# Optimization experiments

Hardware: AMD Instinct MI355X
Metric: run time of the kernel (lower is better)

The kernel has to match this reference:

```python
import jax, jax.numpy as jnp
import numpy as np
import math

B, H, S, D = 4, 16, 2048, 128

def setup_inputs() -> dict:
    key = jax.random.key(0)
    kq, kk, kv = jax.random.split(key, 3)
    query = jax.random.normal(kq, (B, H, S, D), dtype=jnp.float32)
    k = jax.random.normal(kk, (B, H, S, D), dtype=jnp.float32)
    value = jax.random.normal(kv, (B, H, S, D), dtype=jnp.float32)
    attn_mask = jnp.tril(jnp.ones((S, S), dtype=bool))  # causal
    key_padding_mask = jnp.ones((B, S), dtype=bool)      # all keys valid
    return {"query": query, "key": k, "value": value,
            "attn_mask": attn_mask, "key_padding_mask": key_padding_mask}

def reference(query, key, value, attn_mask, key_padding_mask):
    dk = query.shape[-1]
    # [B,H,Sq,Sk]
    scores = jnp.einsum('bhqd,bhkd->bhqk', query, key) / math.sqrt(dk)
    fill = jnp.finfo(scores.dtype).min
    # attn_mask [Sq,Sk] -> [1,1,Sq,Sk]; True = keep
    scores = jnp.where(attn_mask[None, None, :, :], scores, fill)
    # key_padding_mask [B,Sk] -> [B,1,1,Sk]; True = keep
    scores = jnp.where(key_padding_mask[:, None, None, :], scores, fill)
    attn = jax.nn.softmax(scores, axis=-1)
    # dropout p=0.0 / eval mode -> identity
    return jnp.einsum('bhqk,bhkd->bhqd', attn, value)
```

## Files before the change

### kernel.cpp

```cpp
#include <hip/hip_runtime.h>
#include <hip/hip_bf16.h>
#include <math.h>

#define S_LEN 2048
#define D_DIM 128
#define NHEADS 64

typedef unsigned short u16;
typedef __attribute__((ext_vector_type(8))) short bf16x8;
typedef __attribute__((ext_vector_type(4))) float f32x4;
typedef __attribute__((ext_vector_type(16))) float f32x16;

__device__ __forceinline__ u16 f2b(float f) {
  union { float f; unsigned u; } v; v.f = f;
  return (u16)((v.u + 0x7fffu + ((v.u >> 16) & 1u)) >> 16);
}
__device__ __forceinline__ unsigned cvtpk(float lo, float hi) {
  unsigned r;
  asm("v_cvt_pk_bf16_f32 %0, %1, %2" : "=v"(r) : "v"(lo), "v"(hi));
  return r;
}
__device__ __forceinline__ void pl32swap(unsigned &a, unsigned &b) {
  asm("v_permlane32_swap_b32 %0, %1" : "+v"(a), "+v"(b));
}
__device__ __forceinline__ f32x16 z16() {
  f32x16 v;
  #pragma unroll
  for (int i = 0; i < 16; ++i) v[i] = 0.f;
  return v;
}

#define GLL16(g, l) __builtin_amdgcn_global_load_lds(                       \
    (const __attribute__((address_space(1))) unsigned*)(g),                 \
    (__attribute__((address_space(3))) unsigned*)(l), 16, 0, 0)

__global__ __launch_bounds__(256, 2)
void conv_kernel(const float* __restrict__ K, const float* __restrict__ V,
                 u16* __restrict__ Kws, u16* __restrict__ Vws) {
  __shared__ float VLf[128 * 65];
  const int h = blockIdx.x >> 3;
  const int s = blockIdx.x & 7;
  const int tid = threadIdx.x;
  const size_t hb = (size_t)h * S_LEN * D_DIM;
  const float* Kb = K + hb;
  const float* Vb = V + hb;
  u16* Ko = Kws + hb;
  u16* Vo = Vws + hb;

  #pragma unroll 2
  for (int it = 0; it < 16; ++it) {
    int idx = it * 256 + tid;
    int k = 256 * s + (idx >> 4), g = idx & 15;
    const float* src = Kb + (size_t)k * D_DIM + 8 * g;
    float4 a = *(const float4*)src;
    float4 b = *(const float4*)(src + 4);
    bf16x8 f;
    f[0]=f2b(a.x); f[1]=f2b(a.y); f[2]=f2b(a.z); f[3]=f2b(a.w);
    f[4]=f2b(b.x); f[5]=f2b(b.y); f[6]=f2b(b.z); f[7]=f2b(b.w);
    *(bf16x8*)&Ko[(size_t)k * D_DIM + 8 * g] = f;
  }
  for (int tt = 0; tt < 4; ++tt) {
    const int k0t = 256 * s + 64 * tt;
    __syncthreads();
    #pragma unroll 2
    for (int it = 0; it < 8; ++it) {
      int idx = it * 256 + tid;
      int row = idx >> 5, c4 = idx & 31;
      float4 v = *(const float4*)(Vb + (size_t)(k0t + row) * D_DIM + 4 * c4);
      VLf[(4*c4 + 0) * 65 + row] = v.x;
      VLf[(4*c4 + 1) * 65 + row] = v.y;
      VLf[(4*c4 + 2) * 65 + row] = v.z;
      VLf[(4*c4 + 3) * 65 + row] = v.w;
    }
    __syncthreads();
    #pragma unroll
    for (int it = 0; it < 4; ++it) {
      int idx = it * 256 + tid;
      int d = idx >> 3, kc = idx & 7;
      const float* src = &VLf[d * 65 + 8 * kc];
      bf16x8 f;
      #pragma unroll
      for (int j = 0; j < 8; ++j) f[j] = f2b(src[j]);
      *(bf16x8*)&Vo[(size_t)d * S_LEN + k0t + 8 * kc] = f;
    }
  }
}

__global__ __launch_bounds__(512, 2)
void fattn8w(const float* __restrict__ Qg, const u16* __restrict__ Kws,
             const u16* __restrict__ Vws, float* __restrict__ Og) {
  __shared__ __align__(16) u16 Kl[2][8192];
  __shared__ __align__(16) u16 Vl[2][8192];

  const int tid = threadIdx.x, lane = tid & 63, w = tid >> 6;
  const int l31 = lane & 31, hi = lane >> 5;
  const int kx = l31 & 7;

  const int b = blockIdx.x;
  const int xcd = b & 7, slot = b >> 3;
  const int head = xcd * 8 + (slot & 7);
  const int qsel = slot >> 3;
  const int qmap[8] = {7, 5, 6, 4, 0, 2, 1, 3};
  const int qt = qmap[qsel];

  const size_t hb = (size_t)head * S_LEN * D_DIM;
  const float* Qb = Qg + hb;
  float*       Ob = Og + hb;
  const u16*   Kh = Kws + hb;
  const u16*   Vh = Vws + hb;

  auto stage = [&](int buf, int t) {
    const int k0 = t * 64;
    #pragma unroll
    for (int j = 0; j < 2; ++j) {
      const int sb = (w * 2 + j) * 64;
      {
        int sk = sb + lane;
        int k = sk >> 4, gs = sk & 15, g = gs ^ (k & 7);
        GLL16(Kh + (size_t)(k0 + k) * D_DIM + 8 * g, &Kl[buf][sb * 8]);
      }
      {
        int sv = sb + lane;
        int d = sv >> 3, gks = sv & 7, gk = gks ^ (d & 7);
        GLL16(Vh + (size_t)d * S_LEN + k0 + 8 * gk, &Vl[buf][sb * 8]);
      }
    }
  };

#define CHUNK(SV, CB, CI)                                                   \
  do {                                                                      \
    float p0 = exp2f((SV)[(CB)+0] - m_run), p1 = exp2f((SV)[(CB)+1] - m_run); \
    float p2 = exp2f((SV)[(CB)+2] - m_run), p3 = exp2f((SV)[(CB)+3] - m_run); \
    float p4 = exp2f((SV)[(CB)+4] - m_run), p5 = exp2f((SV)[(CB)+5] - m_run); \
    float p6 = exp2f((SV)[(CB)+6] - m_run), p7 = exp2f((SV)[(CB)+7] - m_run); \
    psA += (p0 + p1) + (p2 + p3);                                           \
    psB += (p4 + p5) + (p6 + p7);                                           \
    unsigned a0 = cvtpk(p0, p1), a1 = cvtpk(p2, p3);                        \
    unsigned a2 = cvtpk(p4, p5), a3 = cvtpk(p6, p7);                        \
    pl32swap(a0, a2); pl32swap(a1, a3);                                     \
    union { unsigned u[4]; bf16x8 v; } pf_;                                 \
    pf_.u[0] = a0; pf_.u[1] = a1; pf_.u[2] = a2; pf_.u[3] = a3;             \
    const int gv = ((CI) * 2 + hi) ^ kx;                                    \
    bf16x8 v0 = *(const bf16x8*)&V8[( l31      ) * 64 + gv * 8];            \
    bf16x8 v1 = *(const bf16x8*)&V8[( 32 + l31 ) * 64 + gv * 8];            \
    bf16x8 v2 = *(const bf16x8*)&V8[( 64 + l31 ) * 64 + gv * 8];            \
    bf16x8 v3 = *(const bf16x8*)&V8[( 96 + l31 ) * 64 + gv * 8];            \
    __builtin_amdgcn_s_setprio(1);                                          \
    oa0 = __builtin_amdgcn_mfma_f32_32x32x16_bf16(v0, pf_.v, oa0, 0,0,0);   \
    oa1 = __builtin_amdgcn_mfma_f32_32x32x16_bf16(v1, pf_.v, oa1, 0,0,0);   \
    oa2 = __builtin_amdgcn_mfma_f32_32x32x16_bf16(v2, pf_.v, oa2, 0,0,0);   \
    oa3 = __builtin_amdgcn_mfma_f32_32x32x16_bf16(v3, pf_.v, oa3, 0,0,0);   \
    __builtin_amdgcn_s_setprio(0);                                          \
  } while (0)

  const int q0w = qt * 256 + 32 * w;
  const int ntk = 4 * qt + 4;
  const int myq = q0w + l31;

  stage(0, 0);

  bf16x8 qf[8];
  {
    const float sc = 0.12753139f;
    const float* qp = Qb + (size_t)myq * D_DIM + 8 * hi;
    #pragma unroll
    for (int c = 0; c < 8; ++c) {
      float4 a = *(const float4*)(qp + 16 * c);
      float4 b2 = *(const float4*)(qp + 16 * c + 4);
      bf16x8 f;
      f[0]=f2b(a.x*sc);  f[1]=f2b(a.y*sc);  f[2]=f2b(a.z*sc);  f[3]=f2b(a.w*sc);
      f[4]=f2b(b2.x*sc); f[5]=f2b(b2.y*sc); f[6]=f2b(b2.z*sc); f[7]=f2b(b2.w*sc);
      qf[c] = f;
    }
  }

  f32x16 oa0 = z16(), oa1 = z16(), oa2 = z16(), oa3 = z16();
  float m_run = 0.f, l_run = 0.f;

  #pragma unroll 1
  for (int t = 0; t < ntk; ++t) {
    asm volatile("s_waitcnt vmcnt(0)" ::: "memory");
    __builtin_amdgcn_s_barrier();
    asm volatile("" ::: "memory");
    if (t + 1 < ntk) stage((t + 1) & 1, t + 1);

    if (64 * t <= q0w + 31) {
      const u16* K8 = &Kl[t & 1][0];
      const u16* V8 = &Vl[t & 1][0];

      f32x16 s0 = z16(), s1 = z16();
      __builtin_amdgcn_s_setprio(1);
      #pragma unroll
      for (int c = 0; c < 8; ++c) {
        const int gs = (c * 2 + hi) ^ kx;
        bf16x8 ka = *(const bf16x8*)&K8[ l31       * 128 + gs * 8];
        bf16x8 kb = *(const bf16x8*)&K8[(32 + l31) * 128 + gs * 8];
        s0 = __builtin_amdgcn_mfma_f32_32x32x16_bf16(ka, qf[c], s0, 0,0,0);
        s1 = __builtin_amdgcn_mfma_f32_32x32x16_bf16(kb, qf[c], s1, 0,0,0);
      }
      __builtin_amdgcn_s_setprio(0);

      if (64 * t + 63 > q0w) {
        const int qm = myq - 64 * t;
        #pragma unroll
        for (int i = 0; i < 16; ++i) {
          const int kr = (i & 3) + 8 * (i >> 2) + 4 * hi;
          if (kr > qm)      s0[i] = -1e30f;
          if (32 + kr > qm) s1[i] = -1e30f;
        }
      }

      float tm[16];
      #pragma unroll
      for (int i = 0; i < 16; ++i) tm[i] = fmaxf(s0[i], s1[i]);
      #pragma unroll
      for (int st = 8; st >= 1; st >>= 1)
        #pragma unroll
        for (int i = 0; i < 8; ++i) if (i < st) tm[i] = fmaxf(tm[i], tm[i+st]);
      float mx = fmaxf(tm[0], __shfl_xor(tm[0], 32));

      if (mx > m_run + 8.0f) {
        float corr = exp2f(m_run - mx);
        #pragma unroll
        for (int i = 0; i < 16; ++i) {
          oa0[i] *= corr; oa1[i] *= corr; oa2[i] *= corr; oa3[i] *= corr;
        }
        l_run *= corr; m_run = mx;
      }

      float psA = 0.f, psB = 0.f;
      CHUNK(s0, 0, 0);
      CHUNK(s0, 8, 1);
      CHUNK(s1, 0, 2);
      CHUNK(s1, 8, 3);
      l_run += psA + psB;
    }
  }

  float l_tot = l_run + __shfl_xor(l_run, 32);
  float inv = 1.0f / l_tot;
  float* op = Ob + (size_t)myq * D_DIM;
  #pragma unroll
  for (int bq = 0; bq < 4; ++bq) {
    const int d0 = 8 * bq + 4 * hi;
    *(float4*)(op + d0) =
      make_float4(oa0[4*bq]*inv, oa0[4*bq+1]*inv, oa0[4*bq+2]*inv, oa0[4*bq+3]*inv);
    *(float4*)(op + 32 + d0) =
      make_float4(oa1[4*bq]*inv, oa1[4*bq+1]*inv, oa1[4*bq+2]*inv, oa1[4*bq+3]*inv);
    *(float4*)(op + 64 + d0) =
      make_float4(oa2[4*bq]*inv, oa2[4*bq+1]*inv, oa2[4*bq+2]*inv, oa2[4*bq+3]*inv);
    *(float4*)(op + 96 + d0) =
      make_float4(oa3[4*bq]*inv, oa3[4*bq+1]*inv, oa3[4*bq+2]*inv, oa3[4*bq+3]*inv);
  }
#undef CHUNK
}

__global__ __launch_bounds__(256, 3)
void fattn_v2(const float* __restrict__ Qg, const float* __restrict__ Kg,
              const float* __restrict__ Vg, float* __restrict__ Og) {
  __shared__ __align__(16) u16 K8[16 * 64 * 8];
  __shared__ __align__(16) u16 V8[8 * 128 * 8];
  __shared__ __align__(16) u16 Plf[4 * 16 * 72];
  const int tid = threadIdx.x, lane = tid & 63, w = tid >> 6;
  const int lr = lane & 15, lg = lane >> 4;
  const int qtile = blockIdx.x % 32, bh = blockIdx.x / 32;
  const int q0 = qtile * 64;
  const size_t base = (size_t)bh * S_LEN * D_DIM;
  const float *Qb = Qg + base, *Kb = Kg + base, *Vb = Vg + base;
  float* Ob = Og + base;
  bf16x8 qf[4];
  {
    const float* qp = Qb + (size_t)(q0 + w * 16 + lr) * D_DIM + lg * 8;
    #pragma unroll
    for (int cc = 0; cc < 4; ++cc) {
      float4 a = *(const float4*)(qp + cc * 32);
      float4 b = *(const float4*)(qp + cc * 32 + 4);
      bf16x8 f;
      f[0]=f2b(a.x); f[1]=f2b(a.y); f[2]=f2b(a.z); f[3]=f2b(a.w);
      f[4]=f2b(b.x); f[5]=f2b(b.y); f[6]=f2b(b.z); f[7]=f2b(b.w);
      qf[cc] = f;
    }
  }
  f32x4 oacc[8];
  #pragma unroll
  for (int c = 0; c < 8; ++c) oacc[c] = (f32x4){0.f,0.f,0.f,0.f};
  float m_run[4] = {-INFINITY,-INFINITY,-INFINITY,-INFINITY};
  float l_run[4] = {0.f,0.f,0.f,0.f};
  const int sg_ = tid >> 5, dq_ = tid & 31;
  float4 kb[8], vb[8];
  auto prefetch = [&](int k0) {
    const float* kp = Kb + (size_t)(k0 + lane) * D_DIM;
    #pragma unroll
    for (int i = 0; i < 4; ++i) {
      int dg = w + 4 * i;
      kb[2*i]   = *(const float4*)(kp + dg * 8);
      kb[2*i+1] = *(const float4*)(kp + dg * 8 + 4);
    }
    #pragma unroll
    for (int jj = 0; jj < 8; ++jj) {
      int row = k0 + (jj & 3) * 16 + 2 * sg_ + (jj >> 2);
      vb[jj] = *(const float4*)(Vb + (size_t)row * D_DIM + dq_ * 4);
    }
  };
  const int ntiles = qtile + 1;
  const float scale = 0.08838834764831845f;
  prefetch(0);
  for (int t = 0; t < ntiles; ++t) {
    #pragma unroll
    for (int i = 0; i < 4; ++i) {
      int dg = w + 4 * i;
      float4 a = kb[2*i], b = kb[2*i+1];
      bf16x8 f;
      f[0]=f2b(a.x); f[1]=f2b(a.y); f[2]=f2b(a.z); f[3]=f2b(a.w);
      f[4]=f2b(b.x); f[5]=f2b(b.y); f[6]=f2b(b.z); f[7]=f2b(b.w);
      *(bf16x8*)&K8[(dg * 64 + lane) * 8] = f;
    }
    #pragma unroll
    for (int dd = 0; dd < 4; ++dd) {
      bf16x8 f;
      #pragma unroll
      for (int jj = 0; jj < 8; ++jj) {
        float c = (dd==0)?vb[jj].x:(dd==1)?vb[jj].y:(dd==2)?vb[jj].z:vb[jj].w;
        f[jj] = f2b(c);
      }
      *(bf16x8*)&V8[(sg_ * 128 + dq_ * 4 + dd) * 8] = f;
    }
    __syncthreads();
    if (t + 1 < ntiles) prefetch((t + 1) * 64);
    const bool diag = (t == qtile);
    f32x4 sa[4];
    #pragma unroll
    for (int c = 0; c < 4; ++c) sa[c] = (f32x4){0.f,0.f,0.f,0.f};
    #pragma unroll
    for (int cc = 0; cc < 4; ++cc) {
      #pragma unroll
      for (int c = 0; c < 4; ++c) {
        bf16x8 kf = *(const bf16x8*)&K8[((cc*4+lg)*64 + c*16 + lr)*8];
        sa[c] = __builtin_amdgcn_mfma_f32_16x16x32_bf16(qf[cc], kf, sa[c], 0,0,0);
      }
    }
    #pragma unroll
    for (int r = 0; r < 4; ++r) {
      float s0=sa[0][r]*scale, s1=sa[1][r]*scale, s2=sa[2][r]*scale, s3=sa[3][r]*scale;
      if (diag) {
        int lim = 16*w + lg*4 + r;
        if (     lr > lim) s0 = -INFINITY;
        if (16 + lr > lim) s1 = -INFINITY;
        if (32 + lr > lim) s2 = -INFINITY;
        if (48 + lr > lim) s3 = -INFINITY;
      }
      float mx = fmaxf(fmaxf(s0,s1), fmaxf(s2,s3));
      #pragma unroll
      for (int d = 1; d < 16; d <<= 1) mx = fmaxf(mx, __shfl_xor(mx, d));
      float mn = fmaxf(m_run[r], mx);
      float corr = __expf(m_run[r] - mn);
      float p0=__expf(s0-mn), p1=__expf(s1-mn), p2=__expf(s2-mn), p3=__expf(s3-mn);
      float ps = (p0+p1)+(p2+p3);
      #pragma unroll
      for (int d = 1; d < 16; d <<= 1) ps += __shfl_xor(ps, d);
      l_run[r] = l_run[r]*corr + ps;
      m_run[r] = mn;
      #pragma unroll
      for (int c = 0; c < 8; ++c) oacc[c][r] *= corr;
      ushort4 pw = make_ushort4(f2b(p0), f2b(p1), f2b(p2), f2b(p3));
      *(ushort4*)&Plf[((w*16 + lg*4 + r) * 72) + 4*lr] = pw;
    }
    #pragma unroll
    for (int pass = 0; pass < 2; ++pass) {
      bf16x8 pfv = *(const bf16x8*)&Plf[(w*16 + lr)*72 + pass*32 + lg*8];
      #pragma unroll
      for (int c = 0; c < 8; ++c) {
        bf16x8 vf = *(const bf16x8*)&V8[((pass*4 + lg)*128 + c*16 + lr)*8];
        oacc[c] = __builtin_amdgcn_mfma_f32_16x16x32_bf16(pfv, vf, oacc[c], 0,0,0);
      }
    }
    __syncthreads();
  }
  #pragma unroll
  for (int r = 0; r < 4; ++r) {
    const int mq = q0 + w*16 + lg*4 + r;
    const float inv = 1.0f / l_run[r];
    float* op = Ob + (size_t)mq * D_DIM + lr;
    #pragma unroll
    for (int c = 0; c < 8; ++c) op[c*16] = oacc[c][r] * inv;
  }
}

extern "C" void kernel_launch(void* const* d_in, const int* in_sizes, int n_in,
                              void* d_out, int out_size, void* d_ws, size_t ws_size,
                              hipStream_t stream) {
  const float* Q = (const float*)d_in[0];
  const float* K = (const float*)d_in[1];
  const float* V = (const float*)d_in[2];
  float* O = (float*)d_out;
  const size_t elems = (size_t)NHEADS * S_LEN * D_DIM;
  const size_t need = 2 * elems * sizeof(u16);
  if (ws_size >= need) {
    u16* Kws = (u16*)d_ws;
    u16* Vws = Kws + elems;
    conv_kernel<<<dim3(512), dim3(256), 0, stream>>>(K, V, Kws, Vws);
    fattn8w<<<dim3(512), dim3(512), 0, stream>>>(Q, Kws, Vws, O);
  } else {
    fattn_v2<<<dim3(NHEADS * 32), dim3(256), 0, stream>>>(Q, K, V, O);
  }
}
```

Baseline: 172.4 us.

## Switch flash attention to 4-wave blocks with 32-key tiles

Replaces the 8-wave, 256-query-per-block kernel with a 4-wave kernel covering 128 queries per block, launched as 1024 blocks. Each step now processes 32 keys instead of 64, which halves LDS buffers and lets more blocks share a CU. It also replaces the XCD-aware head mapping with a simpler head index plus a causal-balancing query-tile order. The trade-off is more loop iterations and barriers per key and less K/V reuse per staged tile, and the XCD-local L2 grouping of heads is lost.

New measurement: 365.0 us. 112% more time.

```diff
diff --git a/kernel.cpp b/kernel.cpp
--- a/kernel.cpp
+++ b/kernel.cpp
@@ -86,22 +86,22 @@
   }
 }
 
-__global__ __launch_bounds__(512, 2)
-void fattn8w(const float* __restrict__ Qg, const u16* __restrict__ Kws,
+__global__ __launch_bounds__(256, 4)
+void fattn4w(const float* __restrict__ Qg, const u16* __restrict__ Kws,
              const u16* __restrict__ Vws, float* __restrict__ Og) {
-  __shared__ __align__(16) u16 Kl[2][8192];
-  __shared__ __align__(16) u16 Vl[2][8192];
+  __shared__ __align__(16) u16 Kl[2][4096];
+  __shared__ __align__(16) u16 Vl[2][4096];
 
   const int tid = threadIdx.x, lane = tid & 63, w = tid >> 6;
   const int l31 = lane & 31, hi = lane >> 5;
   const int kx = l31 & 7;
+  const int vx = (l31 >> 1) & 3;
 
   const int b = blockIdx.x;
-  const int xcd = b & 7, slot = b >> 3;
-  const int head = xcd * 8 + (slot & 7);
-  const int qsel = slot >> 3;
-  const int qmap[8] = {7, 5, 6, 4, 0, 2, 1, 3};
-  const int qt = qmap[qsel];
+  const int head = b & 63;
+  const int qsel = b >> 6;
+  const int g = qsel >> 2, i = qsel & 3;
+  const int qt = (g & 1) ? ((g >> 1) + 2 * i) : ((15 - (g >> 1)) - 2 * i);
 
   const size_t hb = (size_t)head * S_LEN * D_DIM;
   const float* Qb = Qg + hb;
@@ -110,24 +110,24 @@
   const u16*   Vh = Vws + hb;
 
   auto stage = [&](int buf, int t) {
-    const int k0 = t * 64;
+    const int k0 = t * 32;
     #pragma unroll
     for (int j = 0; j < 2; ++j) {
       const int sb = (w * 2 + j) * 64;
       {
         int sk = sb + lane;
-        int k = sk >> 4, gs = sk & 15, g = gs ^ (k & 7);
-        GLL16(Kh + (size_t)(k0 + k) * D_DIM + 8 * g, &Kl[buf][sb * 8]);
+        int k = sk >> 4, gs = sk & 15, gg = gs ^ (k & 7);
+        GLL16(Kh + (size_t)(k0 + k) * D_DIM + 8 * gg, &Kl[buf][sb * 8]);
       }
       {
         int sv = sb + lane;
-        int d = sv >> 3, gks = sv & 7, gk = gks ^ (d & 7);
+        int d = sv >> 2, gks = sv & 3, gk = gks ^ ((d >> 1) & 3);
         GLL16(Vh + (size_t)d * S_LEN + k0 + 8 * gk, &Vl[buf][sb * 8]);
       }
     }
   };
 
-#define CHUNK(SV, CB, CI)                                                   \
+#define CHUNK(SV, CB, KC)                                                   \
   do {                                                                      \
     float p0 = exp2f((SV)[(CB)+0] - m_run), p1 = exp2f((SV)[(CB)+1] - m_run); \
     float p2 = exp2f((SV)[(CB)+2] - m_run), p3 = exp2f((SV)[(CB)+3] - m_run); \
@@ -140,11 +140,11 @@
     pl32swap(a0, a2); pl32swap(a1, a3);                                     \
     union { unsigned u[4]; bf16x8 v; } pf_;                                 \
     pf_.u[0] = a0; pf_.u[1] = a1; pf_.u[2] = a2; pf_.u[3] = a3;             \
-    const int gv = ((CI) * 2 + hi) ^ kx;                                    \
-    bf16x8 v0 = *(const bf16x8*)&V8[( l31      ) * 64 + gv * 8];            \
-    bf16x8 v1 = *(const bf16x8*)&V8[( 32 + l31 ) * 64 + gv * 8];            \
-    bf16x8 v2 = *(const bf16x8*)&V8[( 64 + l31 ) * 64 + gv * 8];            \
-    bf16x8 v3 = *(const bf16x8*)&V8[( 96 + l31 ) * 64 + gv * 8];            \
+    const int gv = ((KC) * 2 + hi) ^ vx;                                    \
+    bf16x8 v0 = *(const bf16x8*)&Vl[rb][( l31      ) * 32 + gv * 8];        \
+    bf16x8 v1 = *(const bf16x8*)&Vl[rb][( 32 + l31 ) * 32 + gv * 8];        \
+    bf16x8 v2 = *(const bf16x8*)&Vl[rb][( 64 + l31 ) * 32 + gv * 8];        \
+    bf16x8 v3 = *(const bf16x8*)&Vl[rb][( 96 + l31 ) * 32 + gv * 8];        \
     __builtin_amdgcn_s_setprio(1);                                          \
     oa0 = __builtin_amdgcn_mfma_f32_32x32x16_bf16(v0, pf_.v, oa0, 0,0,0);   \
     oa1 = __builtin_amdgcn_mfma_f32_32x32x16_bf16(v1, pf_.v, oa1, 0,0,0);   \
@@ -153,7 +153,7 @@
     __builtin_amdgcn_s_setprio(0);                                          \
   } while (0)
 
-  const int q0w = qt * 256 + 32 * w;
+  const int q0w = qt * 128 + 32 * w;
   const int ntk = 4 * qt + 4;
   const int myq = q0w + l31;
 
@@ -182,57 +182,50 @@
     asm volatile("s_waitcnt vmcnt(0)" ::: "memory");
     __builtin_amdgcn_s_barrier();
     asm volatile("" ::: "memory");
-    if (t + 1 < ntk) stage((t + 1) & 1, t + 1);
-
-    if (64 * t <= q0w + 31) {
-      const u16* K8 = &Kl[t & 1][0];
-      const u16* V8 = &Vl[t & 1][0];
-
-      f32x16 s0 = z16(), s1 = z16();
+    const int rb = t & 1;
+    if (t + 1 < ntk) stage(rb ^ 1, t + 1);
+
+    if (32 * t <= q0w + 31) {
+      f32x16 s = z16();
       __builtin_amdgcn_s_setprio(1);
       #pragma unroll
       for (int c = 0; c < 8; ++c) {
         const int gs = (c * 2 + hi) ^ kx;
-        bf16x8 ka = *(const bf16x8*)&K8[ l31       * 128 + gs * 8];
-        bf16x8 kb = *(const bf16x8*)&K8[(32 + l31) * 128 + gs * 8];
-        s0 = __builtin_amdgcn_mfma_f32_32x32x16_bf16(ka, qf[c], s0, 0,0,0);
-        s1 = __builtin_amdgcn_mfma_f32_32x32x16_bf16(kb, qf[c], s1, 0,0,0);
+        bf16x8 ka = *(const bf16x8*)&Kl[rb][l31 * 128 + gs * 8];
+        s = __builtin_amdgcn_mfma_f32_32x32x16_bf16(ka, qf[c], s, 0, 0, 0);
       }
       __builtin_amdgcn_s_setprio(0);
 
-      if (64 * t + 63 > q0w) {
-        const int qm = myq - 64 * t;
+      if (32 * t + 31 > q0w) {
+        const int qm = myq - 32 * t;
         #pragma unroll
-        for (int i = 0; i < 16; ++i) {
-          const int kr = (i & 3) + 8 * (i >> 2) + 4 * hi;
-          if (kr > qm)      s0[i] = -1e30f;
-          if (32 + kr > qm) s1[i] = -1e30f;
+        for (int i2 = 0; i2 < 16; ++i2) {
+          const int kr = (i2 & 3) + 8 * (i2 >> 2) + 4 * hi;
+          if (kr > qm) s[i2] = -1e30f;
         }
       }
 
-      float tm[16];
-      #pragma unroll
-      for (int i = 0; i < 16; ++i) tm[i] = fmaxf(s0[i], s1[i]);
-      #pragma unroll
-      for (int st = 8; st >= 1; st >>= 1)
-        #pragma unroll
-        for (int i = 0; i < 8; ++i) if (i < st) tm[i] = fmaxf(tm[i], tm[i+st]);
-      float mx = fmaxf(tm[0], __shfl_xor(tm[0], 32));
+      float t0 = fmaxf(s[0], s[1]),   t1 = fmaxf(s[2], s[3]);
+      float t2 = fmaxf(s[4], s[5]),   t3 = fmaxf(s[6], s[7]);
+      float t4 = fmaxf(s[8], s[9]),   t5 = fmaxf(s[10], s[11]);
+      float t6 = fmaxf(s[12], s[13]), t7 = fmaxf(s[14], s[15]);
+      t0 = fmaxf(fmaxf(t0, t1), fmaxf(t2, t3));
+      t4 = fmaxf(fmaxf(t4, t5), fmaxf(t6, t7));
+      float mx = fmaxf(t0, t4);
+      mx = fmaxf(mx, __shfl_xor(mx, 32));
 
       if (mx > m_run + 8.0f) {
         float corr = exp2f(m_run - mx);
         #pragma unroll
-        for (int i = 0; i < 16; ++i) {
-          oa0[i] *= corr; oa1[i] *= corr; oa2[i] *= corr; oa3[i] *= corr;
+        for (int i2 = 0; i2 < 16; ++i2) {
+          oa0[i2] *= corr; oa1[i2] *= corr; oa2[i2] *= corr; oa3[i2] *= corr;
         }
         l_run *= corr; m_run = mx;
       }
 
       float psA = 0.f, psB = 0.f;
-      CHUNK(s0, 0, 0);
-      CHUNK(s0, 8, 1);
-      CHUNK(s1, 0, 2);
-      CHUNK(s1, 8, 3);
+      CHUNK(s, 0, 0);
+      CHUNK(s, 8, 1);
       l_run += psA + psB;
     }
   }
@@ -399,7 +392,7 @@
     u16* Kws = (u16*)d_ws;
     u16* Vws = Kws + elems;
     conv_kernel<<<dim3(512), dim3(256), 0, stream>>>(K, V, Kws, Vws);
-    fattn8w<<<dim3(512), dim3(512), 0, stream>>>(Q, Kws, Vws, O);
+    fattn4w<<<dim3(1024), dim3(256), 0, stream>>>(Q, Kws, Vws, O);
   } else {
     fattn_v2<<<dim3(NHEADS * 32), dim3(256), 0, stream>>>(Q, K, V, O);
   }
```
